# Kernel optimization log

Measured on AMD Instinct MI355X. Metric: run time of the kernel, lower is better.

## Reference

```python
import jax, jax.numpy as jnp
import numpy as np

B, S, T = 8, 32, 64
V = S * T        # 2048 flattened variables
P = 512          # prediction points
N = 2 * S        # neighbors per prediction point
I = 256          # input_dim
H, AD = 8, 32    # attn_heads, attn_dim
D = H * AD       # 256
M = 256          # mlp hidden dim
L = 2            # attn layers
R = 128          # resolution


def setup_inputs() -> dict:
    ks = iter(jax.random.split(jax.random.key(0), 64))
    def w(shape):
        return jax.random.normal(next(ks), shape, jnp.float32) / np.sqrt(shape[-2])
    inp = {
        "encoded": jax.random.normal(next(ks), (B, V, I), jnp.float32),
        "true_u": jax.random.uniform(next(ks), (B, V, 1), jnp.float32),
        "attn_mask": jnp.zeros((P, N), jnp.float32),
        "pred_points": jnp.sort(jax.random.randint(next(ks), (P,), 0, V)),
        "neighbor_index": jax.random.randint(next(ks), (P, N), 0, V),
    }
    for p in ("k", "v"):
        inp[p + "W1"] = w((L, H, I + 1, M)); inp[p + "b1"] = jnp.zeros((L, H, M))
        inp[p + "W2"] = w((L, H, M, M));     inp[p + "b2"] = jnp.zeros((L, H, M))
        inp[p + "W3"] = w((L, H, M, AD));    inp[p + "b3"] = jnp.zeros((L, H, AD))
    inp["ds_W"] = w((I, D)); inp["ds_b"] = jnp.zeros((D,))
    inp["ln1_g"] = jnp.ones((L, D)); inp["ln1_b"] = jnp.zeros((L, D))
    inp["ff_W1"] = w((L, D, D)); inp["ff_b1"] = jnp.zeros((L, D))
    inp["ff_W2"] = w((L, D, D)); inp["ff_b2"] = jnp.zeros((L, D))
    inp["ln2_g"] = jnp.ones((L, D)); inp["ln2_b"] = jnp.zeros((L, D))
    inp["de_W1"] = w((D, M)); inp["de_b1"] = jnp.zeros((M,))
    inp["de_W2"] = w((M, M)); inp["de_b2"] = jnp.zeros((M,))
    inp["de_W3"] = w((M, R)); inp["de_b3"] = jnp.zeros((R,))
    return inp


def _ln(x, g, b):
    mu = x.mean(-1, keepdims=True)
    var = ((x - mu) ** 2).mean(-1, keepdims=True)
    return (x - mu) * jax.lax.rsqrt(var + 1e-5) * g + b


def _kv(x, W1, b1, W2, b2, W3, b3):
    # x: [B,V,I+1]; W1: [L,H,I+1,M] -> per-layer per-head MLP, out [L,B,H,V,AD]
    h = jax.nn.relu(jnp.einsum('bvi,lhim->lbhvm', x, W1) + b1[:, None, :, None, :])
    h = jax.nn.relu(jnp.einsum('lbhvm,lhmn->lbhvn', h, W2) + b2[:, None, :, None, :])
    return jnp.einsum('lbhvm,lhmd->lbhvd', h, W3) + b3[:, None, :, None, :]


def _forward(encoded, true_u, attn_mask, kW1, kb1, kW2, kb2, kW3, kb3,
             vW1, vb1, vW2, vb2, vW3, vb3, ds_W, ds_b, ln1_g, ln1_b,
             ff_W1, ff_b1, ff_W2, ff_b2, ln2_g, ln2_b,
             de_W1, de_b1, de_W2, de_b2, de_W3, de_b3,
             pred_points, neighbor_index):
    attn_dim = kW3.shape[-1]
    n_heads = kW1.shape[1]
    merged = jnp.concatenate([encoded, true_u], axis=-1)        # [B,V,I+1]
    keys = _kv(merged, kW1, kb1, kW2, kb2, kW3, kb3)            # [L,B,H,V,d]
    vals = _kv(merged, vW1, vb1, vW2, vb2, vW3, vb3)            # [L,B,H,V,d]

    cur = encoded[:, pred_points, :]                            # [B,P,I]
    att_value = cur @ ds_W + ds_b                               # [B,P,D]
    nb, np_, dd = att_value.shape
    scale = attn_dim ** (-0.5)
    for l in range(keys.shape[0]):
        q = att_value.reshape(nb, np_, n_heads, attn_dim)       # [B,P,H,d]
        nk = keys[l][:, :, neighbor_index, :]                   # [B,H,P,N,d]
        nv = vals[l][:, :, neighbor_index, :]                   # [B,H,P,N,d]
        scores = (jnp.einsum('bphd,bhpnd->bphn', q, nk) - attn_mask[None, :, None, :]) * scale
        wts = jax.nn.softmax(scores, axis=-1)                   # [B,P,H,N]
        att = jnp.einsum('bphn,bhpnd->bphd', wts, nv).reshape(nb, np_, dd)
        att_value = _ln(att_value + att, ln1_g[l], ln1_b[l])
        ff = jax.nn.relu(att_value @ ff_W1[l] + ff_b1[l]) @ ff_W2[l] + ff_b2[l]
        att_value = _ln(att_value + ff, ln2_g[l], ln2_b[l])

    h = jax.nn.relu(att_value @ de_W1 + de_b1)
    h = jax.nn.relu(h @ de_W2 + de_b2)
    logits = h @ de_W3 + de_b3                                  # [B,P,R]
    res = logits.shape[-1]
    target = jnp.clip(jnp.floor(true_u * res).astype(jnp.int32), 0, res - 1)
    target = target[:, pred_points, :]                          # [B,P,1]
    logprob = jnp.log(jnp.float32(res)) + jax.nn.log_softmax(logits, axis=-1)
    picked = jnp.take_along_axis(logprob, target, axis=2)       # [B,P,1]
    return -picked.sum((1, 2))                                  # [B]


def reference(encoded, true_u, attn_mask, kW1, kb1, kW2, kb2, kW3, kb3,
              vW1, vb1, vW2, vb2, vW3, vb3, ds_W, ds_b, ln1_g, ln1_b,
              ff_W1, ff_b1, ff_W2, ff_b2, ln2_g, ln2_b,
              de_W1, de_b1, de_W2, de_b2, de_W3, de_b3,
              pred_points, neighbor_index):
    return _forward(encoded, true_u, attn_mask, kW1, kb1, kW2, kb2, kW3, kb3,
                    vW1, vb1, vW2, vb2, vW3, vb3, ds_W, ds_b, ln1_g, ln1_b,
                    ff_W1, ff_b1, ff_W2, ff_b2, ln2_g, ln2_b,
                    de_W1, de_b1, de_W2, de_b2, de_W3, de_b3,
                    pred_points, neighbor_index)
```

## Files before the change

kernel.cpp:

```cpp
#include <hip/hip_runtime.h>
#include <hip/hip_bf16.h>
#include <cstdint>
#include <cstddef>

constexpr int Bc = 8;
constexpr int Vc = 2048;
constexpr int Pc = 512;
constexpr int Hc = 8;
constexpr int Lc = 2;
constexpr int ROWS_KV = Bc * Vc;
constexpr int ROWS_AT = Bc * Pc;

typedef __attribute__((ext_vector_type(8))) short bf16x8;
typedef __attribute__((ext_vector_type(4))) float f32x4;

static __device__ __forceinline__ unsigned short f2bf(float v) {
    __hip_bfloat16 h = __float2bfloat16(v);
    return *(unsigned short*)&h;
}
static __device__ __forceinline__ float bflo(unsigned int u) {
    return __uint_as_float(u << 16);
}
static __device__ __forceinline__ float bfhi(unsigned int u) {
    return __uint_as_float(u & 0xffff0000u);
}

__global__ __launch_bounds__(256) void prep_all_kernel(
    const float* kW1, const float* vW1, const float* kW2, const float* vW2,
    const float* kW3, const float* vW3,
    const float* ds_W, const float* ff_W1, const float* ff_W2,
    const float* de_W1, const float* de_W2, const float* de_W3,
    const float* encoded,
    unsigned short* __restrict__ W1t, unsigned short* __restrict__ W2t,
    unsigned short* __restrict__ W3t, unsigned short* __restrict__ Wm,
    unsigned short* __restrict__ Xbf)
{
    const int z = blockIdx.z;
    if (z >= 104) {
        const int idx = (z - 104) * 64 + blockIdx.y * 8 + blockIdx.x;
        if (idx >= 4096) return;
        const int i = idx * 256 + threadIdx.x;
        float4 v = ((const float4*)encoded)[i];
        ushort4 o;
        o.x = f2bf(v.x); o.y = f2bf(v.y); o.z = f2bf(v.z); o.w = f2bf(v.w);
        ((ushort4*)Xbf)[i] = o;
        return;
    }
    const float* src;
    unsigned short* dst;
    int C;
    if (z < 32) {
        const int net = z;
        src = ((net >> 4) ? vW1 : kW1) + (size_t)(net & 15) * 257 * 256;
        dst = W1t + (size_t)net * 65536;
        C = 256;
    } else if (z < 64) {
        const int net = z - 32;
        src = ((net >> 4) ? vW2 : kW2) + (size_t)(net & 15) * 256 * 256;
        dst = W2t + (size_t)net * 65536;
        C = 256;
    } else if (z < 96) {
        const int net = z - 64;
        src = ((net >> 4) ? vW3 : kW3) + (size_t)(net & 15) * 256 * 32;
        dst = W3t + (size_t)net * 8192;
        C = 32;
    } else {
        const int id = z - 96;
        const float* srcs[8] = {ds_W, ff_W1, ff_W1 + (size_t)65536,
                                ff_W2, ff_W2 + (size_t)65536, de_W1, de_W2, de_W3};
        src = srcs[id];
        dst = Wm + (size_t)id * 65536;
        C = (id == 7) ? 128 : 256;
    }
    if (blockIdx.x * 32 >= C) return;
    __shared__ float t[32][33];
    const int c0 = blockIdx.x * 32, k0 = blockIdx.y * 32;
    const int tx = threadIdx.x & 31, ty = threadIdx.x >> 5;
    #pragma unroll
    for (int i = 0; i < 32; i += 8)
        t[ty + i][tx] = src[(size_t)(k0 + ty + i) * C + (c0 + tx)];
    __syncthreads();
    #pragma unroll
    for (int i = 0; i < 32; i += 8)
        dst[(size_t)(c0 + ty + i) * 256 + (k0 + tx)] = f2bf(t[tx][ty + i]);
}

static __device__ __forceinline__ int hsw_chunk(int row, int ks, int quad) {
    int c = ks * 4 + quad;
    int p = c ^ (row & 31);
    return row * 256 + p * 8;
}
static __device__ __forceinline__ int hsw_elem(int row, int col) {
    int p = (col >> 3) ^ (row & 31);
    return row * 256 + p * 8 + (col & 7);
}
static __device__ __forceinline__ int hsw_b64(int row, int col0) {
    int c = col0 >> 3;
    return row * 256 + ((c ^ (row & 31)) * 8) + (col0 & 7);
}

__global__ __launch_bounds__(512, 2) void kv_mfma_kernel(
    const unsigned short* __restrict__ Xbf, const float* __restrict__ true_u,
    const unsigned short* __restrict__ W1t, const unsigned short* __restrict__ W2t,
    const unsigned short* __restrict__ W3t,
    const float* __restrict__ kW1, const float* __restrict__ vW1,
    const float* __restrict__ kb1, const float* __restrict__ kb2, const float* __restrict__ kb3,
    const float* __restrict__ vb1, const float* __restrict__ vb2, const float* __restrict__ vb3,
    unsigned short* __restrict__ keys, unsigned short* __restrict__ vals)
{
    __shared__ unsigned short buf0[64 * 256];
    __shared__ unsigned short buf1[64 * 256];
    __shared__ unsigned short w3buf[32 * 256];
    __shared__ float tub[2][64];

    const int tid = threadIdx.x;
    const int w = tid >> 6, lane = tid & 63;
    const int ln = lane & 15, quad = lane >> 4;
    const int lh = blockIdx.y, isv = blockIdx.z;
    const int net = isv * 16 + lh;
    const float* W1f = (isv ? vW1 : kW1) + (size_t)lh * 257 * 256;
    const float* b1  = (isv ? vb1 : kb1) + lh * 256;
    const float* b2  = (isv ? vb2 : kb2) + lh * 256;
    const float* b3  = (isv ? vb3 : kb3) + lh * 32;
    const unsigned short* w1 = W1t + (size_t)net * 65536;
    const unsigned short* w2 = W2t + (size_t)net * 65536;
    const unsigned short* w3 = W3t + (size_t)net * 8192;
    unsigned short* outp = isv ? vals : keys;
    const int base = blockIdx.x * 1024;
    const int cb = w * 32;

    bf16x8 B1[16], B2[16];
    {
        const unsigned short* p1 = w1 + (size_t)(cb + ln) * 256 + quad * 8;
        const unsigned short* p2 = w2 + (size_t)(cb + ln) * 256 + quad * 8;
        #pragma unroll
        for (int ks = 0; ks < 8; ++ks)
            #pragma unroll
            for (int ct = 0; ct < 2; ++ct) {
                B1[ks * 2 + ct] = *(const bf16x8*)(p1 + (size_t)ct * 16 * 256 + ks * 32);
                B2[ks * 2 + ct] = *(const bf16x8*)(p2 + (size_t)ct * 16 * 256 + ks * 32);
            }
    }
    {
        #pragma unroll
        for (int j = 0; j < 2; ++j) {
            const int cidx = tid * 2 + j;
            const int col = cidx >> 5, c = cidx & 31;
            uint4 d = *(const uint4*)(w3 + cidx * 8);
            *(uint4*)&w3buf[col * 256 + (c ^ (col & 31)) * 8] = d;
        }
    }
    float4 b1v4[2], b2v4[2], w1f4[2];
    #pragma unroll
    for (int ct = 0; ct < 2; ++ct) {
        const int col = cb + ct * 16 + quad * 4;
        b1v4[ct] = *(const float4*)(b1 + col);
        b2v4[ct] = *(const float4*)(b2 + col);
        w1f4[ct] = *(const float4*)(W1f + 256 * 256 + col);
    }
    const int rt3 = w & 3, ct3 = w >> 2;
    const float4 b3v4 = *(const float4*)(b3 + ct3 * 16 + quad * 4);

    const int b_ = base >> 11;
    const int l_ = lh >> 3, h_ = lh & 7;
    unsigned short* ob = outp + (((size_t)l_ * Bc + b_) * Vc) * 256 + h_ * 32;

    const f32x4 zero = {0.f, 0.f, 0.f, 0.f};
    const int xr = tid >> 3, cg = tid & 7;

    {
        const unsigned short* gx = Xbf + (size_t)(base + xr) * 256;
        #pragma unroll
        for (int j = 0; j < 4; ++j) {
            const int c = j * 8 + cg;
            uint4 d = *(const uint4*)(gx + c * 8);
            *(uint4*)&buf0[xr * 256 + ((c ^ (xr & 31)) * 8)] = d;
        }
        if (tid < 64) tub[0][tid] = true_u[base + tid];
    }
    __syncthreads();

    unsigned short* bufX = buf0;
    unsigned short* bufH = buf1;

    for (int t = 0; t < 16; ++t) {
        const int row0 = base + t * 64;

        f32x4 acc[4][2];
        #pragma unroll
        for (int rt = 0; rt < 4; ++rt) { acc[rt][0] = zero; acc[rt][1] = zero; }
        {
            bf16x8 A[4], An[4];
            #pragma unroll
            for (int rt = 0; rt < 4; ++rt)
                A[rt] = *(const bf16x8*)&bufX[hsw_chunk(rt * 16 + ln, 0, quad)];
            #pragma unroll
            for (int ks = 0; ks < 8; ++ks) {
                if (ks < 7) {
                    #pragma unroll
                    for (int rt = 0; rt < 4; ++rt)
                        An[rt] = *(const bf16x8*)&bufX[hsw_chunk(rt * 16 + ln, ks + 1, quad)];
                }
                #pragma unroll
                for (int rt = 0; rt < 4; ++rt)
                    #pragma unroll
                    for (int ct = 0; ct < 2; ++ct)
                        acc[rt][ct] = __builtin_amdgcn_mfma_f32_16x16x32_bf16(
                            B1[ks * 2 + ct], A[rt], acc[rt][ct], 0, 0, 0);
                if (ks < 7) {
                    #pragma unroll
                    for (int rt = 0; rt < 4; ++rt) A[rt] = An[rt];
                }
            }
        }
        #pragma unroll
        for (int rt = 0; rt < 4; ++rt) {
            const int row = rt * 16 + ln;
            const float tu = tub[t & 1][row];
            #pragma unroll
            for (int ct = 0; ct < 2; ++ct) {
                const int col0 = cb + ct * 16 + quad * 4;
                ushort4 o;
                o.x = f2bf(fmaxf(acc[rt][ct][0] + b1v4[ct].x + tu * w1f4[ct].x, 0.f));
                o.y = f2bf(fmaxf(acc[rt][ct][1] + b1v4[ct].y + tu * w1f4[ct].y, 0.f));
                o.z = f2bf(fmaxf(acc[rt][ct][2] + b1v4[ct].z + tu * w1f4[ct].z, 0.f));
                o.w = f2bf(fmaxf(acc[rt][ct][3] + b1v4[ct].w + tu * w1f4[ct].w, 0.f));
                *(ushort4*)&bufH[hsw_b64(row, col0)] = o;
            }
        }
        __syncthreads();

        uint4 xp[4];
        float tun = 0.f;
        const bool havex = (t < 15);
        if (havex) {
            const unsigned short* gx = Xbf + (size_t)(row0 + 64 + xr) * 256;
            #pragma unroll
            for (int j = 0; j < 4; ++j)
                xp[j] = *(const uint4*)(gx + (j * 8 + cg) * 8);
            if (tid < 64) tun = true_u[row0 + 64 + tid];
        }

        #pragma unroll
        for (int rt = 0; rt < 4; ++rt) { acc[rt][0] = zero; acc[rt][1] = zero; }
        #pragma unroll
        for (int ks = 0; ks < 8; ++ks) {
            bf16x8 A[4];
            #pragma unroll
            for (int rt = 0; rt < 4; ++rt)
                A[rt] = *(const bf16x8*)&bufH[hsw_chunk(rt * 16 + ln, ks, quad)];
            #pragma unroll
            for (int rt = 0; rt < 4; ++rt)
                #pragma unroll
                for (int ct = 0; ct < 2; ++ct)
                    acc[rt][ct] = __builtin_amdgcn_mfma_f32_16x16x32_bf16(
                        B2[ks * 2 + ct], A[rt], acc[rt][ct], 0, 0, 0);
        }
        #pragma unroll
        for (int rt = 0; rt < 4; ++rt) {
            const int row = rt * 16 + ln;
            #pragma unroll
            for (int ct = 0; ct < 2; ++ct) {
                const int col0 = cb + ct * 16 + quad * 4;
                ushort4 o;
                o.x = f2bf(fmaxf(acc[rt][ct][0] + b2v4[ct].x, 0.f));
                o.y = f2bf(fmaxf(acc[rt][ct][1] + b2v4[ct].y, 0.f));
                o.z = f2bf(fmaxf(acc[rt][ct][2] + b2v4[ct].z, 0.f));
                o.w = f2bf(fmaxf(acc[rt][ct][3] + b2v4[ct].w, 0.f));
                *(ushort4*)&bufX[hsw_b64(row, col0)] = o;
            }
        }
        __syncthreads();

        if (havex) {
            #pragma unroll
            for (int j = 0; j < 4; ++j) {
                const int c = j * 8 + cg;
                *(uint4*)&bufH[xr * 256 + ((c ^ (xr & 31)) * 8)] = xp[j];
            }
            if (tid < 64) tub[(t + 1) & 1][tid] = tun;
        }

        f32x4 acc3 = zero;
        #pragma unroll
        for (int ks = 0; ks < 8; ++ks) {
            bf16x8 Aw = *(const bf16x8*)&w3buf[hsw_chunk(ct3 * 16 + ln, ks, quad)];
            bf16x8 Ah = *(const bf16x8*)&bufX[hsw_chunk(rt3 * 16 + ln, ks, quad)];
            acc3 = __builtin_amdgcn_mfma_f32_16x16x32_bf16(Aw, Ah, acc3, 0, 0, 0);
        }
        {
            const int grow = row0 + rt3 * 16 + ln;
            ushort4 o;
            o.x = f2bf(acc3[0] + b3v4.x);
            o.y = f2bf(acc3[1] + b3v4.y);
            o.z = f2bf(acc3[2] + b3v4.z);
            o.w = f2bf(acc3[3] + b3v4.w);
            *(ushort4*)(ob + (size_t)(grow & 2047) * 256 + ct3 * 16 + quad * 4) = o;
        }
        __syncthreads();

        unsigned short* tmp = bufX; bufX = bufH; bufH = tmp;
    }
}

__global__ __launch_bounds__(512) void decoder_kernel(
    const unsigned short* __restrict__ Xbf, const float* __restrict__ true_u,
    const unsigned short* __restrict__ keys, const unsigned short* __restrict__ vals,
    const int* __restrict__ nbr, const float* __restrict__ mask,
    const int* __restrict__ pp, const unsigned short* __restrict__ Wm,
    const float* __restrict__ ds_b,
    const float* __restrict__ ln1_g, const float* __restrict__ ln1_b,
    const float* __restrict__ ff_b1, const float* __restrict__ ff_b2,
    const float* __restrict__ ln2_g, const float* __restrict__ ln2_b,
    const float* __restrict__ de_b1, const float* __restrict__ de_b2,
    const float* __restrict__ de_b3, float* __restrict__ outp)
{
    __shared__ float avF[16][264];
    __shared__ float attF[16][264];
    __shared__ unsigned short abuf[16 * 256];
    __shared__ unsigned short hbuf[16 * 256];
    __shared__ int   ni_s[16][64];
    __shared__ float wtsb[16][64];
    __shared__ float psum[16][8], psq[16][8];
    __shared__ float rowmax[16];
    __shared__ int   tcol[16];
    __shared__ int   pps[16];

    const int tid = threadIdx.x;
    const int w = tid >> 6, lane = tid & 63;
    const int ln = lane & 15, quad = lane >> 4;
    const int bid = blockIdx.x;
    const int b = bid & 7;
    const int r0 = b * 512 + (bid >> 3) * 16;
    const int cb = w * 32;

    const f32x4 zero = {0.f, 0.f, 0.f, 0.f};

    if (tid < 16) pps[tid] = pp[(r0 + tid) & 511];
    #pragma unroll
    for (int j = 0; j < 2; ++j) {
        const int idx = tid * 2 + j;
        const int row = idx >> 6, n = idx & 63;
        ni_s[row][n] = nbr[((r0 + row) & 511) * 64 + n];
    }
    __syncthreads();

    {
        const int row = tid >> 5, c = tid & 31;
        const size_t arow = (size_t)b * Vc + pps[row];
        uint4 d = *(const uint4*)(Xbf + arow * 256 + c * 8);
        *(uint4*)&abuf[row * 256 + ((c ^ row) * 8)] = d;
    }
    __syncthreads();

    {
        const unsigned short* Wt = Wm;
        f32x4 acc[2]; acc[0] = zero; acc[1] = zero;
        const unsigned short* wb = Wt + (size_t)(cb + ln) * 256 + quad * 8;
        #pragma unroll
        for (int ks = 0; ks < 8; ++ks) {
            bf16x8 A = *(const bf16x8*)&abuf[hsw_chunk(ln, ks, quad)];
            #pragma unroll
            for (int ct = 0; ct < 2; ++ct) {
                bf16x8 Bv = *(const bf16x8*)(wb + (size_t)ct * 16 * 256 + ks * 32);
                acc[ct] = __builtin_amdgcn_mfma_f32_16x16x32_bf16(A, Bv, acc[ct], 0, 0, 0);
            }
        }
        __syncthreads();
        #pragma unroll
        for (int ct = 0; ct < 2; ++ct) {
            const int col = cb + ct * 16 + ln;
            const float bb = ds_b[col];
            #pragma unroll
            for (int r = 0; r < 4; ++r) {
                const int row = quad * 4 + r;
                float v = acc[ct][r] + bb;
                avF[row][col] = v;
                abuf[hsw_elem(row, col)] = f2bf(v);
            }
        }
    }
    __syncthreads();

    for (int l = 0; l < Lc; ++l) {
        const unsigned short* kvb = keys + (((size_t)l * Bc + b) * Vc) * 256;
        const unsigned short* vvb = vals + (((size_t)l * Bc + b) * Vc) * 256;

        {
            const int row0a = w * 2, row1a = w * 2 + 1;
            const int p0 = (r0 + row0a) & 511, p1 = (r0 + row1a) & 511;
            const int n = lane;
            const int vi0 = ni_s[row0a][n], vi1 = ni_s[row1a][n];
            const float m0 = mask[p0 * 64 + n], m1 = mask[p1 * 64 + n];
            const int nb4 = n >> 2, cg8 = (n & 3) * 8;
            int vrow0[4], vrow1[4];
            #pragma unroll
            for (int pass = 0; pass < 4; ++pass) {
                const int nn = pass * 16 + nb4;
                vrow0[pass] = ni_s[row0a][nn];
                vrow1[pass] = ni_s[row1a][nn];
            }
            for (int h = 0; h < 8; ++h) {
                uint4 vu0[4], vu1[4];
                #pragma unroll
                for (int pass = 0; pass < 4; ++pass) {
                    vu0[pass] = *(const uint4*)(vvb + (size_t)vrow0[pass] * 256 + h * 32 + cg8);
                    vu1[pass] = *(const uint4*)(vvb + (size_t)vrow1[pass] * 256 + h * 32 + cg8);
                }
                float q0[32], q1[32];
                #pragma unroll
                for (int j = 0; j < 8; ++j) {
                    float4 t0 = *(const float4*)&avF[row0a][h * 32 + j * 4];
                    float4 t1 = *(const float4*)&avF[row1a][h * 32 + j * 4];
                    q0[j * 4 + 0] = t0.x; q0[j * 4 + 1] = t0.y;
                    q0[j * 4 + 2] = t0.z; q0[j * 4 + 3] = t0.w;
                    q1[j * 4 + 0] = t1.x; q1[j * 4 + 1] = t1.y;
                    q1[j * 4 + 2] = t1.z; q1[j * 4 + 3] = t1.w;
                }
                const unsigned short* kp0 = kvb + (size_t)vi0 * 256 + h * 32;
                const unsigned short* kp1 = kvb + (size_t)vi1 * 256 + h * 32;
                float s0 = 0.f, s1 = 0.f;
                #pragma unroll
                for (int j = 0; j < 4; ++j) {
                    uint4 u0 = *(const uint4*)(kp0 + j * 8);
                    uint4 u1 = *(const uint4*)(kp1 + j * 8);
                    s0 += q0[j * 8 + 0] * bflo(u0.x) + q0[j * 8 + 1] * bfhi(u0.x);
                    s1 += q1[j * 8 + 0] * bflo(u1.x) + q1[j * 8 + 1] * bfhi(u1.x);
                    s0 += q0[j * 8 + 2] * bflo(u0.y) + q0[j * 8 + 3] * bfhi(u0.y);
                    s1 += q1[j * 8 + 2] * bflo(u1.y) + q1[j * 8 + 3] * bfhi(u1.y);
                    s0 += q0[j * 8 + 4] * bflo(u0.z) + q0[j * 8 + 5] * bfhi(u0.z);
                    s1 += q1[j * 8 + 4] * bflo(u1.z) + q1[j * 8 + 5] * bfhi(u1.z);
                    s0 += q0[j * 8 + 6] * bflo(u0.w) + q0[j * 8 + 7] * bfhi(u0.w);
                    s1 += q1[j * 8 + 6] * bflo(u1.w) + q1[j * 8 + 7] * bfhi(u1.w);
                }
                s0 = (s0 - m0) * 0.17677669529663689f;
                s1 = (s1 - m1) * 0.17677669529663689f;
                float mx0 = s0, mx1 = s1;
                #pragma unroll
                for (int off = 32; off >= 1; off >>= 1) {
                    mx0 = fmaxf(mx0, __shfl_xor(mx0, off));
                    mx1 = fmaxf(mx1, __shfl_xor(mx1, off));
                }
                float e0 = expf(s0 - mx0), e1 = expf(s1 - mx1);
                float sum0 = e0, sum1 = e1;
                #pragma unroll
                for (int off = 32; off >= 1; off >>= 1) {
                    sum0 += __shfl_xor(sum0, off);
                    sum1 += __shfl_xor(sum1, off);
                }
                wtsb[row0a][n] = e0 / sum0;
                wtsb[row1a][n] = e1 / sum1;
                float a0[8], a1[8];
                #pragma unroll
                for (int j = 0; j < 8; ++j) { a0[j] = 0.f; a1[j] = 0.f; }
                #pragma unroll
                for (int pass = 0; pass < 4; ++pass) {
                    const int nn = pass * 16 + nb4;
                    const float w0 = wtsb[row0a][nn], w1 = wtsb[row1a][nn];
                    uint4 u0 = vu0[pass];
                    uint4 u1 = vu1[pass];
                    a0[0] += w0 * bflo(u0.x); a0[1] += w0 * bfhi(u0.x);
                    a1[0] += w1 * bflo(u1.x); a1[1] += w1 * bfhi(u1.x);
                    a0[2] += w0 * bflo(u0.y); a0[3] += w0 * bfhi(u0.y);
                    a1[2] += w1 * bflo(u1.y); a1[3] += w1 * bfhi(u1.y);
                    a0[4] += w0 * bflo(u0.z); a0[5] += w0 * bfhi(u0.z);
                    a1[4] += w1 * bflo(u1.z); a1[5] += w1 * bfhi(u1.z);
                    a0[6] += w0 * bflo(u0.w); a0[7] += w0 * bfhi(u0.w);
                    a1[6] += w1 * bflo(u1.w); a1[7] += w1 * bfhi(u1.w);
                }
                #pragma unroll
                for (int off = 4; off <= 32; off <<= 1)
                    #pragma unroll
                    for (int j = 0; j < 8; ++j) {
                        a0[j] += __shfl_xor(a0[j], off);
                        a1[j] += __shfl_xor(a1[j], off);
                    }
                if (nb4 == 0)
                    #pragma unroll
                    for (int j = 0; j < 8; ++j) {
                        attF[row0a][h * 32 + cg8 + j] = a0[j];
                        attF[row1a][h * 32 + cg8 + j] = a1[j];
                    }
            }
            #pragma unroll
            for (int rr = 0; rr < 2; ++rr) {
                const int row = w * 2 + rr;
                const int c0 = lane * 4;
                float x[4];
                float sl = 0.f, ql = 0.f;
                #pragma unroll
                for (int j = 0; j < 4; ++j) {
                    x[j] = avF[row][c0 + j] + attF[row][c0 + j];
                    sl += x[j]; ql += x[j] * x[j];
                }
                #pragma unroll
                for (int off = 32; off >= 1; off >>= 1) {
                    sl += __shfl_xor(sl, off);
                    ql += __shfl_xor(ql, off);
                }
                const float mu = sl * (1.0f / 256.0f);
                const float var = ql * (1.0f / 256.0f) - mu * mu;
                const float rstd = 1.0f / sqrtf(fmaxf(var, 0.f) + 1e-5f);
                #pragma unroll
                for (int j = 0; j < 4; ++j) {
                    const int col = c0 + j;
                    float o = (x[j] - mu) * rstd * ln1_g[l * 256 + col] + ln1_b[l * 256 + col];
                    avF[row][col] = o;
                    abuf[hsw_elem(row, col)] = f2bf(o);
                }
            }
        }
        __syncthreads();

        {
            const unsigned short* W1 = Wm + (size_t)(1 + l) * 65536;
            f32x4 acc[2]; acc[0] = zero; acc[1] = zero;
            const unsigned short* wb = W1 + (size_t)(cb + ln) * 256 + quad * 8;
            #pragma unroll
            for (int ks = 0; ks < 8; ++ks) {
                bf16x8 A = *(const bf16x8*)&abuf[hsw_chunk(ln, ks, quad)];
                #pragma unroll
                for (int ct = 0; ct < 2; ++ct) {
                    bf16x8 Bv = *(const bf16x8*)(wb + (size_t)ct * 16 * 256 + ks * 32);
                    acc[ct] = __builtin_amdgcn_mfma_f32_16x16x32_bf16(A, Bv, acc[ct], 0, 0, 0);
                }
            }
            #pragma unroll
            for (int ct = 0; ct < 2; ++ct) {
                const int col = cb + ct * 16 + ln;
                const float bb = ff_b1[l * 256 + col];
                #pragma unroll
                for (int r = 0; r < 4; ++r) {
                    const int row = quad * 4 + r;
                    hbuf[hsw_elem(row, col)] = f2bf(fmaxf(acc[ct][r] + bb, 0.f));
                }
            }
        }
        __syncthreads();

        {
            const unsigned short* W2 = Wm + (size_t)(3 + l) * 65536;
            f32x4 acc[2]; acc[0] = zero; acc[1] = zero;
            const unsigned short* wb = W2 + (size_t)(cb + ln) * 256 + quad * 8;
            #pragma unroll
            for (int ks = 0; ks < 8; ++ks) {
                bf16x8 A = *(const bf16x8*)&hbuf[hsw_chunk(ln, ks, quad)];
                #pragma unroll
                for (int ct = 0; ct < 2; ++ct) {
                    bf16x8 Bv = *(const bf16x8*)(wb + (size_t)ct * 16 * 256 + ks * 32);
                    acc[ct] = __builtin_amdgcn_mfma_f32_16x16x32_bf16(A, Bv, acc[ct], 0, 0, 0);
                }
            }
            float vv[2][4];
            #pragma unroll
            for (int ct = 0; ct < 2; ++ct) {
                const int col = cb + ct * 16 + ln;
                const float bb = ff_b2[l * 256 + col];
                #pragma unroll
                for (int r = 0; r < 4; ++r) {
                    const int row = quad * 4 + r;
                    vv[ct][r] = acc[ct][r] + bb + avF[row][col];
                }
            }
            #pragma unroll
            for (int r = 0; r < 4; ++r) {
                float sl = vv[0][r] + vv[1][r];
                float ql = vv[0][r] * vv[0][r] + vv[1][r] * vv[1][r];
                #pragma unroll
                for (int off = 8; off >= 1; off >>= 1) {
                    sl += __shfl_xor(sl, off);
                    ql += __shfl_xor(ql, off);
                }
                if (ln == 0) {
                    const int row = quad * 4 + r;
                    psum[row][w] = sl; psq[row][w] = ql;
                }
            }
            __syncthreads();
            #pragma unroll
            for (int r = 0; r < 4; ++r) {
                const int row = quad * 4 + r;
                float sl = 0.f, ql = 0.f;
                #pragma unroll
                for (int j = 0; j < 8; ++j) { sl += psum[row][j]; ql += psq[row][j]; }
                const float mu = sl * (1.0f / 256.0f);
                const float var = ql * (1.0f / 256.0f) - mu * mu;
                const float rstd = 1.0f / sqrtf(fmaxf(var, 0.f) + 1e-5f);
                #pragma unroll
                for (int ct = 0; ct < 2; ++ct) {
                    const int col = cb + ct * 16 + ln;
                    float o = (vv[ct][r] - mu) * rstd * ln2_g[l * 256 + col] + ln2_b[l * 256 + col];
                    avF[row][col] = o;
                    abuf[hsw_elem(row, col)] = f2bf(o);
                }
            }
        }
        __syncthreads();
    }

    {
        const unsigned short* W1 = Wm + (size_t)5 * 65536;
        f32x4 acc[2]; acc[0] = zero; acc[1] = zero;
        const unsigned short* wb = W1 + (size_t)(cb + ln) * 256 + quad * 8;
        #pragma unroll
        for (int ks = 0; ks < 8; ++ks) {
            bf16x8 A = *(const bf16x8*)&abuf[hsw_chunk(ln, ks, quad)];
            #pragma unroll
            for (int ct = 0; ct < 2; ++ct) {
                bf16x8 Bv = *(const bf16x8*)(wb + (size_t)ct * 16 * 256 + ks * 32);
                acc[ct] = __builtin_amdgcn_mfma_f32_16x16x32_bf16(A, Bv, acc[ct], 0, 0, 0);
            }
        }
        #pragma unroll
        for (int ct = 0; ct < 2; ++ct) {
            const int col = cb + ct * 16 + ln;
            const float bb = de_b1[col];
            #pragma unroll
            for (int r = 0; r < 4; ++r) {
                const int row = quad * 4 + r;
                hbuf[hsw_elem(row, col)] = f2bf(fmaxf(acc[ct][r] + bb, 0.f));
            }
        }
    }
    __syncthreads();

    {
        const unsigned short* W2 = Wm + (size_t)6 * 65536;
        f32x4 acc[2]; acc[0] = zero; acc[1] = zero;
        const unsigned short* wb = W2 + (size_t)(cb + ln) * 256 + quad * 8;
        #pragma unroll
        for (int ks = 0; ks < 8; ++ks) {
            bf16x8 A = *(const bf16x8*)&hbuf[hsw_chunk(ln, ks, quad)];
            #pragma unroll
            for (int ct = 0; ct < 2; ++ct) {
                bf16x8 Bv = *(const bf16x8*)(wb + (size_t)ct * 16 * 256 + ks * 32);
                acc[ct] = __builtin_amdgcn_mfma_f32_16x16x32_bf16(A, Bv, acc[ct], 0, 0, 0);
            }
        }
        __syncthreads();
        #pragma unroll
        for (int ct = 0; ct < 2; ++ct) {
            const int col = cb + ct * 16 + ln;
            const float bb = de_b2[col];
            #pragma unroll
            for (int r = 0; r < 4; ++r) {
                const int row = quad * 4 + r;
                hbuf[hsw_elem(row, col)] = f2bf(fmaxf(acc[ct][r] + bb, 0.f));
            }
        }
    }
    __syncthreads();

    {
        const unsigned short* W3 = Wm + (size_t)7 * 65536;
        const int cb3 = w * 16;
        f32x4 a3 = zero;
        const unsigned short* wb = W3 + (size_t)(cb3 + ln) * 256 + quad * 8;
        #pragma unroll
        for (int ks = 0; ks < 8; ++ks) {
            bf16x8 A = *(const bf16x8*)&hbuf[hsw_chunk(ln, ks, quad)];
            bf16x8 Bv = *(const bf16x8*)(wb + ks * 32);
            a3 = __builtin_amdgcn_mfma_f32_16x16x32_bf16(A, Bv, a3, 0, 0, 0);
        }
        float lg[4];
        const float bb = de_b3[cb3 + ln];
        #pragma unroll
        for (int r = 0; r < 4; ++r) lg[r] = a3[r] + bb;

        #pragma unroll
        for (int r = 0; r < 4; ++r) {
            float m = lg[r];
            #pragma unroll
            for (int off = 8; off >= 1; off >>= 1) m = fmaxf(m, __shfl_xor(m, off));
            if (ln == 0) psum[quad * 4 + r][w] = m;
        }
        __syncthreads();
        if (tid < 16) {
            float m = psum[tid][0];
            #pragma unroll
            for (int j = 1; j < 8; ++j) m = fmaxf(m, psum[tid][j]);
            rowmax[tid] = m;
            float tu = true_u[(size_t)b * Vc + pps[tid]];
            int t = (int)floorf(tu * 128.0f);
            tcol[tid] = t < 0 ? 0 : (t > 127 ? 127 : t);
        }
        __syncthreads();
        #pragma unroll
        for (int r = 0; r < 4; ++r) {
            const int row = quad * 4 + r;
            const float mx = rowmax[row];
            const int t = tcol[row];
            float e = expf(lg[r] - mx);
            float xt = ((cb3 + ln) == t) ? lg[r] : 0.f;
            #pragma unroll
            for (int off = 8; off >= 1; off >>= 1) {
                e += __shfl_xor(e, off);
                xt += __shfl_xor(xt, off);
            }
            if (ln == 0) { psum[row][w] = e; psq[row][w] = xt; }
        }
        __syncthreads();
        float contrib = 0.f;
        if (tid < 16) {
            float sum = 0.f, xt = 0.f;
            #pragma unroll
            for (int j = 0; j < 8; ++j) { sum += psum[tid][j]; xt += psq[tid][j]; }
            const float lp = logf(128.0f) + (xt - rowmax[tid]) - logf(sum);
            contrib = -lp;
        }
        if (w == 0) {
            #pragma unroll
            for (int off = 32; off >= 1; off >>= 1) contrib += __shfl_xor(contrib, off);
            if (lane == 0) atomicAdd(&outp[b], contrib);
        }
    }
}

extern "C" void kernel_launch(void* const* d_in, const int* in_sizes, int n_in,
                              void* d_out, int out_size, void* d_ws, size_t ws_size,
                              hipStream_t stream)
{
    (void)in_sizes; (void)n_in; (void)out_size; (void)ws_size;

    const float* encoded        = (const float*)d_in[0];
    const float* true_u         = (const float*)d_in[1];
    const float* attn_mask      = (const float*)d_in[2];
    const int*   pred_points    = (const int*)d_in[3];
    const int*   neighbor_index = (const int*)d_in[4];
    const float* kW1 = (const float*)d_in[5];
    const float* kb1 = (const float*)d_in[6];
    const float* kW2 = (const float*)d_in[7];
    const float* kb2 = (const float*)d_in[8];
    const float* kW3 = (const float*)d_in[9];
    const float* kb3 = (const float*)d_in[10];
    const float* vW1 = (const float*)d_in[11];
    const float* vb1 = (const float*)d_in[12];
    const float* vW2 = (const float*)d_in[13];
    const float* vb2 = (const float*)d_in[14];
    const float* vW3 = (const float*)d_in[15];
    const float* vb3 = (const float*)d_in[16];
    const float* ds_W  = (const float*)d_in[17];
    const float* ds_b  = (const float*)d_in[18];
    const float* ln1_g = (const float*)d_in[19];
    const float* ln1_b = (const float*)d_in[20];
    const float* ff_W1 = (const float*)d_in[21];
    const float* ff_b1 = (const float*)d_in[22];
    const float* ff_W2 = (const float*)d_in[23];
    const float* ff_b2 = (const float*)d_in[24];
    const float* ln2_g = (const float*)d_in[25];
    const float* ln2_b = (const float*)d_in[26];
    const float* de_W1 = (const float*)d_in[27];
    const float* de_b1 = (const float*)d_in[28];
    const float* de_W2 = (const float*)d_in[29];
    const float* de_b2 = (const float*)d_in[30];
    const float* de_W3 = (const float*)d_in[31];
    const float* de_b3 = (const float*)d_in[32];

    float* out = (float*)d_out;

    constexpr size_t KV_ELEMS = (size_t)Lc * Bc * Hc * Vc * 32;
    unsigned short* keys = (unsigned short*)d_ws;
    unsigned short* vals = keys + KV_ELEMS;
    unsigned short* Xbf  = vals + KV_ELEMS;
    unsigned short* W1t  = Xbf + (size_t)ROWS_KV * 256;
    unsigned short* W2t  = W1t + (size_t)32 * 65536;
    unsigned short* W3t  = W2t + (size_t)32 * 65536;
    unsigned short* Wm   = W3t + (size_t)32 * 8192;

    (void)hipMemsetAsync(out, 0, Bc * sizeof(float), stream);

    prep_all_kernel<<<dim3(8, 8, 168), 256, 0, stream>>>(
        kW1, vW1, kW2, vW2, kW3, vW3,
        ds_W, ff_W1, ff_W2, de_W1, de_W2, de_W3, encoded,
        W1t, W2t, W3t, Wm, Xbf);

    kv_mfma_kernel<<<dim3(16, 16, 2), 512, 0, stream>>>(
        Xbf, true_u, W1t, W2t, W3t, kW1, vW1,
        kb1, kb2, kb3, vb1, vb2, vb3, keys, vals);

    decoder_kernel<<<dim3(ROWS_AT / 16), 512, 0, stream>>>(
        Xbf, true_u, keys, vals, neighbor_index, attn_mask, pred_points, Wm,
        ds_b, ln1_g, ln1_b, ff_b1, ff_b2, ln2_g, ln2_b,
        de_b1, de_b2, de_b3, out);
}
```

Measured before the change: 445.9 us.

## Replace block barriers in KV MLP with per-wave LDS flags and staggered K order

Swaps the three __syncthreads per tile in the KV MLP kernel for per-wave progress flags in shared memory (flagH, flagG, s1rd) and a third LDS buffer. Each wave starts its layer-2 and layer-3 K loop at its own slice and spin-waits only on the wave that produces the next chunk, so waves can overlap stages instead of all stopping at a barrier. The layer-2 weight registers are reordered to match the staggered order, and the next-tile X prefetch moves earlier. This adds 32KB of LDS, which may limit the two-blocks-per-CU occupancy, and relies on volatile spin loops with fake data dependencies for ordering, which is fragile.

```diff
diff --git a/kernel.cpp b/kernel.cpp
--- a/kernel.cpp
+++ b/kernel.cpp
@@ -108,10 +108,14 @@
     const float* __restrict__ vb1, const float* __restrict__ vb2, const float* __restrict__ vb3,
     unsigned short* __restrict__ keys, unsigned short* __restrict__ vals)
 {
-    __shared__ unsigned short buf0[64 * 256];
-    __shared__ unsigned short buf1[64 * 256];
+    __shared__ unsigned short bufA[64 * 256];
+    __shared__ unsigned short bufB[64 * 256];
+    __shared__ unsigned short bufC[64 * 256];
     __shared__ unsigned short w3buf[32 * 256];
     __shared__ float tub[2][64];
+    __shared__ volatile int flagH[8];
+    __shared__ volatile int flagG[8];
+    __shared__ volatile int s1rd[8];
 
     const int tid = threadIdx.x;
     const int w = tid >> 6, lane = tid & 63;
@@ -129,17 +133,22 @@
     const int base = blockIdx.x * 1024;
     const int cb = w * 32;
 
-    bf16x8 B1[16], B2[16];
+    bf16x8 B1[16], B2r[16];
     {
         const unsigned short* p1 = w1 + (size_t)(cb + ln) * 256 + quad * 8;
         const unsigned short* p2 = w2 + (size_t)(cb + ln) * 256 + quad * 8;
         #pragma unroll
         for (int ks = 0; ks < 8; ++ks)
             #pragma unroll
-            for (int ct = 0; ct < 2; ++ct) {
+            for (int ct = 0; ct < 2; ++ct)
                 B1[ks * 2 + ct] = *(const bf16x8*)(p1 + (size_t)ct * 16 * 256 + ks * 32);
-                B2[ks * 2 + ct] = *(const bf16x8*)(p2 + (size_t)ct * 16 * 256 + ks * 32);
-            }
+        #pragma unroll
+        for (int j = 0; j < 8; ++j) {
+            const int ks = (w + j) & 7;
+            #pragma unroll
+            for (int ct = 0; ct < 2; ++ct)
+                B2r[j * 2 + ct] = *(const bf16x8*)(p2 + (size_t)ct * 16 * 256 + ks * 32);
+        }
     }
     {
         #pragma unroll
@@ -168,20 +177,19 @@
     const f32x4 zero = {0.f, 0.f, 0.f, 0.f};
     const int xr = tid >> 3, cg = tid & 7;
 
+    if (tid < 8) { flagH[tid] = -1; flagG[tid] = -1; s1rd[tid] = -1; }
+
     {
         const unsigned short* gx = Xbf + (size_t)(base + xr) * 256;
         #pragma unroll
         for (int j = 0; j < 4; ++j) {
             const int c = j * 8 + cg;
             uint4 d = *(const uint4*)(gx + c * 8);
-            *(uint4*)&buf0[xr * 256 + ((c ^ (xr & 31)) * 8)] = d;
+            *(uint4*)&bufA[xr * 256 + ((c ^ (xr & 31)) * 8)] = d;
         }
         if (tid < 64) tub[0][tid] = true_u[base + tid];
     }
     __syncthreads();
-
-    unsigned short* bufX = buf0;
-    unsigned short* bufH = buf1;
 
     for (int t = 0; t < 16; ++t) {
         const int row0 = base + t * 64;
@@ -193,13 +201,13 @@
             bf16x8 A[4], An[4];
             #pragma unroll
             for (int rt = 0; rt < 4; ++rt)
-                A[rt] = *(const bf16x8*)&bufX[hsw_chunk(rt * 16 + ln, 0, quad)];
+                A[rt] = *(const bf16x8*)&bufA[hsw_chunk(rt * 16 + ln, 0, quad)];
             #pragma unroll
             for (int ks = 0; ks < 8; ++ks) {
                 if (ks < 7) {
                     #pragma unroll
                     for (int rt = 0; rt < 4; ++rt)
-                        An[rt] = *(const bf16x8*)&bufX[hsw_chunk(rt * 16 + ln, ks + 1, quad)];
+                        An[rt] = *(const bf16x8*)&bufA[hsw_chunk(rt * 16 + ln, ks + 1, quad)];
                 }
                 #pragma unroll
                 for (int rt = 0; rt < 4; ++rt)
@@ -213,6 +221,20 @@
                 }
             }
         }
+        __asm__ volatile("s_waitcnt lgkmcnt(0)" ::: "memory");
+        s1rd[w] = t;
+
+        uint4 xp[4];
+        float tun = 0.f;
+        const bool havex = (t < 15);
+        if (havex) {
+            const unsigned short* gx = Xbf + (size_t)(row0 + 64 + xr) * 256;
+            #pragma unroll
+            for (int j = 0; j < 4; ++j)
+                xp[j] = *(const uint4*)(gx + (j * 8 + cg) * 8);
+            if (tid < 64) tun = true_u[row0 + 64 + tid];
+        }
+
         #pragma unroll
         for (int rt = 0; rt < 4; ++rt) {
             const int row = rt * 16 + ln;
@@ -225,36 +247,33 @@
                 o.y = f2bf(fmaxf(acc[rt][ct][1] + b1v4[ct].y + tu * w1f4[ct].y, 0.f));
                 o.z = f2bf(fmaxf(acc[rt][ct][2] + b1v4[ct].z + tu * w1f4[ct].z, 0.f));
                 o.w = f2bf(fmaxf(acc[rt][ct][3] + b1v4[ct].w + tu * w1f4[ct].w, 0.f));
-                *(ushort4*)&bufH[hsw_b64(row, col0)] = o;
-            }
-        }
-        __syncthreads();
-
-        uint4 xp[4];
-        float tun = 0.f;
-        const bool havex = (t < 15);
-        if (havex) {
-            const unsigned short* gx = Xbf + (size_t)(row0 + 64 + xr) * 256;
-            #pragma unroll
-            for (int j = 0; j < 4; ++j)
-                xp[j] = *(const uint4*)(gx + (j * 8 + cg) * 8);
-            if (tid < 64) tun = true_u[row0 + 64 + tid];
-        }
+                *(ushort4*)&bufB[hsw_b64(row, col0)] = o;
+            }
+        }
+        __asm__ volatile("s_waitcnt lgkmcnt(0)" ::: "memory");
+        flagH[w] = t;
 
         #pragma unroll
         for (int rt = 0; rt < 4; ++rt) { acc[rt][0] = zero; acc[rt][1] = zero; }
         #pragma unroll
-        for (int ks = 0; ks < 8; ++ks) {
+        for (int j = 0; j < 8; ++j) {
+            const int ks = (w + j) & 7;
+            int d0 = 0;
+            if (j) {
+                int fv = flagH[ks];
+                while (fv < t) fv = flagH[ks];
+                __asm__("v_and_b32 %0, 0, %1" : "=v"(d0) : "v"(fv));
+            }
             bf16x8 A[4];
             #pragma unroll
             for (int rt = 0; rt < 4; ++rt)
-                A[rt] = *(const bf16x8*)&bufH[hsw_chunk(rt * 16 + ln, ks, quad)];
+                A[rt] = *(const bf16x8*)&bufB[hsw_chunk(rt * 16 + ln, ks, quad) + d0];
             #pragma unroll
             for (int rt = 0; rt < 4; ++rt)
                 #pragma unroll
                 for (int ct = 0; ct < 2; ++ct)
                     acc[rt][ct] = __builtin_amdgcn_mfma_f32_16x16x32_bf16(
-                        B2[ks * 2 + ct], A[rt], acc[rt][ct], 0, 0, 0);
+                        B2r[j * 2 + ct], A[rt], acc[rt][ct], 0, 0, 0);
         }
         #pragma unroll
         for (int rt = 0; rt < 4; ++rt) {
@@ -267,25 +286,42 @@
                 o.y = f2bf(fmaxf(acc[rt][ct][1] + b2v4[ct].y, 0.f));
                 o.z = f2bf(fmaxf(acc[rt][ct][2] + b2v4[ct].z, 0.f));
                 o.w = f2bf(fmaxf(acc[rt][ct][3] + b2v4[ct].w, 0.f));
-                *(ushort4*)&bufX[hsw_b64(row, col0)] = o;
-            }
-        }
-        __syncthreads();
+                *(ushort4*)&bufC[hsw_b64(row, col0)] = o;
+            }
+        }
+        __asm__ volatile("s_waitcnt lgkmcnt(0)" ::: "memory");
+        flagG[w] = t;
 
         if (havex) {
-            #pragma unroll
-            for (int j = 0; j < 4; ++j) {
-                const int c = j * 8 + cg;
-                *(uint4*)&bufH[xr * 256 + ((c ^ (xr & 31)) * 8)] = xp[j];
+            int accf = 0;
+            #pragma unroll
+            for (int j = 0; j < 8; ++j) {
+                int fv = s1rd[j];
+                while (fv < t) fv = s1rd[j];
+                accf |= fv;
+            }
+            int d1 = 0;
+            __asm__("v_and_b32 %0, 0, %1" : "=v"(d1) : "v"(accf));
+            #pragma unroll
+            for (int j2 = 0; j2 < 4; ++j2) {
+                const int c = j2 * 8 + cg;
+                *(uint4*)&bufA[xr * 256 + ((c ^ (xr & 31)) * 8) + d1] = xp[j2];
             }
             if (tid < 64) tub[(t + 1) & 1][tid] = tun;
         }
 
         f32x4 acc3 = zero;
         #pragma unroll
-        for (int ks = 0; ks < 8; ++ks) {
+        for (int j = 0; j < 8; ++j) {
+            const int ks = (w + j) & 7;
+            int d0 = 0;
+            if (j) {
+                int fv = flagG[ks];
+                while (fv < t) fv = flagG[ks];
+                __asm__("v_and_b32 %0, 0, %1" : "=v"(d0) : "v"(fv));
+            }
             bf16x8 Aw = *(const bf16x8*)&w3buf[hsw_chunk(ct3 * 16 + ln, ks, quad)];
-            bf16x8 Ah = *(const bf16x8*)&bufX[hsw_chunk(rt3 * 16 + ln, ks, quad)];
+            bf16x8 Ah = *(const bf16x8*)&bufC[hsw_chunk(rt3 * 16 + ln, ks, quad) + d0];
             acc3 = __builtin_amdgcn_mfma_f32_16x16x32_bf16(Aw, Ah, acc3, 0, 0, 0);
         }
         {
@@ -297,9 +333,10 @@
             o.w = f2bf(acc3[3] + b3v4.w);
             *(ushort4*)(ob + (size_t)(grow & 2047) * 256 + ct3 * 16 + quad * 4) = o;
         }
-        __syncthreads();
-
-        unsigned short* tmp = bufX; bufX = bufH; bufH = tmp;
+
+        __asm__ volatile("s_waitcnt lgkmcnt(0)" ::: "memory");
+        __builtin_amdgcn_s_barrier();
+        __builtin_amdgcn_sched_barrier(0);
     }
 }
 
```

After: 1.173 ms. +163.0%, slower.
